# Optimization experiments

Hardware: AMD Instinct MI355X
Metric: run time of the kernel (lower is better)

Reference implementation:

```python
import jax, jax.numpy as jnp
import numpy as np

SIZE = 7  # grid size; H = W = SIZE


def setup_inputs() -> dict:
    key = jax.random.key(0)
    k1, k2, k3, k4 = jax.random.split(key, 4)
    N, C = 256, 2048
    x = jax.random.normal(k1, (N, C, SIZE, SIZE), dtype=jnp.float32)
    mask = jax.random.uniform(k2, (N, SIZE, SIZE), dtype=jnp.float32)
    W = jax.random.normal(k3, (2, 2 * C), dtype=jnp.float32) * 0.02
    b = jax.random.normal(k4, (2,), dtype=jnp.float32) * 0.02
    return {"x": x, "mask": mask, "W": W, "b": b}


def reference(x, mask, W, b):
    N, C, H, Wd = x.shape
    HW = H * Wd
    size = float(H)
    # (N, HW, C) tokens
    reduced_x = jnp.transpose(x.reshape(N, C, HW), (0, 2, 1))
    m = mask.reshape(N, HW)
    thr = jnp.mean(m, axis=1, keepdims=True)  # curr_coef = 1.0
    binary_mask = (m > thr).astype(x.dtype)  # (N, HW)
    # mean over channels of masked tokens, then argmax over positions
    masked_mean = jnp.mean(reduced_x * binary_mask[:, :, None], axis=-1)  # (N, HW)
    max_index = jnp.argmax(masked_mean, axis=-1)  # (N,)
    batch_idx = jnp.arange(N)
    max_features = reduced_x[batch_idx, max_index]  # (N, C)
    # concat(max_feature, token) -> tiny linear 2C -> 2 with ReLU
    disc = jnp.concatenate(
        [jnp.broadcast_to(max_features[:, None, :], (N, HW, C)), reduced_x], axis=-1
    )  # (N, HW, 2C)
    preds_coord = jax.nn.relu(jnp.einsum('npc,oc->npo', disc, W) + b)  # (N, HW, 2)
    # zero out prediction at the anchor position
    preds_coord = preds_coord.at[batch_idx, max_index].set(0.0)
    # polar-coordinate targets relative to anchor
    ii, jj = jnp.meshgrid(jnp.arange(H), jnp.arange(Wd), indexing='ij')
    label = jnp.stack([ii, jj], axis=-1).astype(x.dtype).reshape(HW, 2)  # (HW, 2)
    basic_anchor = label[max_index][:, None, :]  # (N, 1, 2)
    rel = (label[None, :, :] - basic_anchor) / size  # (N, HW, 2)
    relative_dist = jnp.sqrt(jnp.sum(rel ** 2, axis=-1))  # (N, HW)
    relative_angle = jnp.arctan2(rel[:, :, 1], rel[:, :, 0])
    relative_angle = (relative_angle / jnp.float32(np.pi) + 1.0) / 2.0  # (N, HW)
    preds_dist = preds_coord[:, :, 0]
    preds_angle = preds_coord[:, :, 1]
    dist_loss = (preds_dist - relative_dist) ** 2
    gap = preds_angle - relative_angle
    gap = jnp.where(gap < 0, gap + 1.0, gap)
    gap = gap - jnp.mean(gap, axis=-1, keepdims=True)
    angle_loss = gap ** 2
    return (dist_loss + angle_loss).reshape(N, H, Wd)
```

## Files before the change

kernel.cpp:

```cpp
#include <hip/hip_runtime.h>
#include <math.h>

#define N_     256
#define C_     2048
#define HW_    49
#define CHUNKS 4
#define CPB    (C_/CHUNKS)
#define CPW    (CPB/4)
#define NG     5

__global__ __launch_bounds__(256) void k_dot(const float* __restrict__ x,
                                             const float* __restrict__ Wm,
                                             float* __restrict__ part) {
  const int chunk = blockIdx.x;
  const int n     = blockIdx.y;
  const int t     = threadIdx.x;
  const int w     = t >> 6;
  const int l     = t & 63;

  __shared__ float red[4][NG][HW_ + 7];

  const int cbase = chunk*CPB + w*CPW;
  const float* xq   = x + ((size_t)n*C_ + cbase)*HW_ + (l < HW_ ? l : 0);
  const float* w_u0 = Wm + cbase;
  const float* w_u1 = Wm + 2*C_ + cbase;
  const float* w_t0 = Wm + C_ + cbase;
  const float* w_t1 = Wm + 3*C_ + cbase;

  float a0=0.f, a1=0.f, a2=0.f, a3=0.f, a4=0.f;
  #pragma unroll 8
  for (int c = 0; c < CPW; ++c) {
    const float xv = xq[(size_t)c*HW_];
    const float b0 = w_u0[c];
    const float b1 = w_u1[c];
    const float b2 = w_t0[c];
    const float b3 = w_t1[c];
    a0 += xv;
    a1 = fmaf(xv, b0, a1);
    a2 = fmaf(xv, b1, a2);
    a3 = fmaf(xv, b2, a3);
    a4 = fmaf(xv, b3, a4);
  }

  if (l < HW_) {
    red[w][0][l] = a0; red[w][1][l] = a1; red[w][2][l] = a2;
    red[w][3][l] = a3; red[w][4][l] = a4;
  }
  __syncthreads();

  if (t < NG*HW_) {
    const int g = t / HW_, p = t - g*HW_;
    const float s = red[0][g][p] + red[1][g][p] + red[2][g][p] + red[3][g][p];
    part[((size_t)n*CHUNKS + chunk)*(NG*HW_) + t] = s;
  }
}

__global__ __launch_bounds__(256) void k_final(const float* __restrict__ part,
                                               const float* __restrict__ mask,
                                               const float* __restrict__ b,
                                               float* __restrict__ out) {
  const int n = blockIdx.x;
  const int t = threadIdx.x;
  __shared__ float red[NG*HW_];

  if (t < NG*HW_) {
    float a = 0.f;
    #pragma unroll
    for (int ch = 0; ch < CHUNKS; ++ch)
      a += part[((size_t)n*CHUNKS + ch)*(NG*HW_) + t];
    red[t] = a;
  }
  __syncthreads();

  if (t < 64) {
    const int  p   = t;
    const bool act = (p < HW_);

    float m = act ? mask[n*HW_ + p] : 0.f;
    float tot = m;
    #pragma unroll
    for (int off = 32; off; off >>= 1) tot += __shfl_xor(tot, off);
    const float thr = tot / 49.f;

    float s  = act ? red[0*HW_ + p] : 0.f;
    float mm = act ? ((m > thr) ? (s * (1.f/2048.f)) : 0.f) : -INFINITY;
    float best = mm;
    int   bidx = act ? p : 64;
    #pragma unroll
    for (int off = 32; off; off >>= 1) {
      float ov = __shfl_xor(best, off);
      int   oi = __shfl_xor(bidx, off);
      if (ov > best || (ov == best && oi < bidx)) { best = ov; bidx = oi; }
    }
    const int mi = bidx;

    const float u0mi = red[1*HW_ + mi];
    const float u1mi = red[2*HW_ + mi];

    float pred0 = 0.f, pred1 = 0.f;
    if (act) {
      pred0 = fmaxf(u0mi + red[3*HW_ + p] + b[0], 0.f);
      pred1 = fmaxf(u1mi + red[4*HW_ + p] + b[1], 0.f);
      if (p == mi) { pred0 = 0.f; pred1 = 0.f; }
    }

    const int ii = p / 7,  jj = p - ii*7;
    const int ai = mi / 7, aj = mi - ai*7;
    const float ri = (float)(ii - ai) / 7.f;
    const float rj = (float)(jj - aj) / 7.f;
    const float dist = sqrtf(ri*ri + rj*rj);
    const float ang  = (atan2f(rj, ri) / 3.14159274101257324f + 1.f) * 0.5f;

    float gap = pred1 - ang;
    if (gap < 0.f) gap += 1.f;
    float gsum = act ? gap : 0.f;
    #pragma unroll
    for (int off = 32; off; off >>= 1) gsum += __shfl_xor(gsum, off);
    const float gmean = gsum / 49.f;

    if (act) {
      const float dl = pred0 - dist;
      const float ga = gap - gmean;
      out[n*HW_ + p] = dl*dl + ga*ga;
    }
  }
}

extern "C" void kernel_launch(void* const* d_in, const int* in_sizes, int n_in,
                              void* d_out, int out_size, void* d_ws, size_t ws_size,
                              hipStream_t stream) {
  const float* x    = (const float*)d_in[0];
  const float* mask = (const float*)d_in[1];
  const float* Wm   = (const float*)d_in[2];
  const float* b    = (const float*)d_in[3];
  float* out  = (float*)d_out;
  float* part = (float*)d_ws;

  dim3 g1(CHUNKS, N_);
  k_dot<<<g1, 256, 0, stream>>>(x, Wm, part);
  k_final<<<N_, 256, 0, stream>>>(part, mask, b, out);
}
```

Baseline: 167.3 us.

## Fuse dot-product and finalize kernels into one 1024-thread block per sample

Merges the two-kernel pipeline into a single kernel with one 1024-thread block per sample. Sixteen waves split the channels and reduce through shared memory, so the global partial-sum buffer and the second launch go away. The trade-off is fewer blocks (256 instead of 1024), which may lower memory-level parallelism across the GPU for this bandwidth-bound read of x.

```diff
diff --git a/kernel.cpp b/kernel.cpp
--- a/kernel.cpp
+++ b/kernel.cpp
@@ -4,23 +4,25 @@
 #define N_     256
 #define C_     2048
 #define HW_    49
-#define CHUNKS 4
-#define CPB    (C_/CHUNKS)
-#define CPW    (CPB/4)
+#define WAVES  16
+#define CPW    (C_/WAVES)
 #define NG     5
+#define LDW    52
 
-__global__ __launch_bounds__(256) void k_dot(const float* __restrict__ x,
-                                             const float* __restrict__ Wm,
-                                             float* __restrict__ part) {
-  const int chunk = blockIdx.x;
-  const int n     = blockIdx.y;
-  const int t     = threadIdx.x;
-  const int w     = t >> 6;
-  const int l     = t & 63;
+__global__ __launch_bounds__(1024) void k_fused(const float* __restrict__ x,
+                                                const float* __restrict__ mask,
+                                                const float* __restrict__ Wm,
+                                                const float* __restrict__ bias,
+                                                float* __restrict__ out) {
+  const int n = blockIdx.x;
+  const int t = threadIdx.x;
+  const int w = t >> 6;
+  const int l = t & 63;
 
-  __shared__ float red[4][NG][HW_ + 7];
+  __shared__ float red[WAVES][NG][LDW];
+  __shared__ float fin[NG][HW_];
 
-  const int cbase = chunk*CPB + w*CPW;
+  const int cbase = w * CPW;
   const float* xq   = x + ((size_t)n*C_ + cbase)*HW_ + (l < HW_ ? l : 0);
   const float* w_u0 = Wm + cbase;
   const float* w_u1 = Wm + 2*C_ + cbase;
@@ -28,7 +30,7 @@
   const float* w_t1 = Wm + 3*C_ + cbase;
 
   float a0=0.f, a1=0.f, a2=0.f, a3=0.f, a4=0.f;
-  #pragma unroll 8
+  #pragma unroll 16
   for (int c = 0; c < CPW; ++c) {
     const float xv = xq[(size_t)c*HW_];
     const float b0 = w_u0[c];
@@ -50,25 +52,10 @@
 
   if (t < NG*HW_) {
     const int g = t / HW_, p = t - g*HW_;
-    const float s = red[0][g][p] + red[1][g][p] + red[2][g][p] + red[3][g][p];
-    part[((size_t)n*CHUNKS + chunk)*(NG*HW_) + t] = s;
-  }
-}
-
-__global__ __launch_bounds__(256) void k_final(const float* __restrict__ part,
-                                               const float* __restrict__ mask,
-                                               const float* __restrict__ b,
-                                               float* __restrict__ out) {
-  const int n = blockIdx.x;
-  const int t = threadIdx.x;
-  __shared__ float red[NG*HW_];
-
-  if (t < NG*HW_) {
-    float a = 0.f;
+    float s = 0.f;
     #pragma unroll
-    for (int ch = 0; ch < CHUNKS; ++ch)
-      a += part[((size_t)n*CHUNKS + ch)*(NG*HW_) + t];
-    red[t] = a;
+    for (int j = 0; j < WAVES; ++j) s += red[j][g][p];
+    fin[g][p] = s;
   }
   __syncthreads();
 
@@ -82,7 +69,7 @@
     for (int off = 32; off; off >>= 1) tot += __shfl_xor(tot, off);
     const float thr = tot / 49.f;
 
-    float s  = act ? red[0*HW_ + p] : 0.f;
+    float s  = act ? fin[0][p] : 0.f;
     float mm = act ? ((m > thr) ? (s * (1.f/2048.f)) : 0.f) : -INFINITY;
     float best = mm;
     int   bidx = act ? p : 64;
@@ -94,13 +81,13 @@
     }
     const int mi = bidx;
 
-    const float u0mi = red[1*HW_ + mi];
-    const float u1mi = red[2*HW_ + mi];
+    const float u0mi = fin[1][mi];
+    const float u1mi = fin[2][mi];
 
     float pred0 = 0.f, pred1 = 0.f;
     if (act) {
-      pred0 = fmaxf(u0mi + red[3*HW_ + p] + b[0], 0.f);
-      pred1 = fmaxf(u1mi + red[4*HW_ + p] + b[1], 0.f);
+      pred0 = fmaxf(u0mi + fin[3][p] + bias[0], 0.f);
+      pred1 = fmaxf(u1mi + fin[4][p] + bias[1], 0.f);
       if (p == mi) { pred0 = 0.f; pred1 = 0.f; }
     }
 
@@ -133,10 +120,7 @@
   const float* mask = (const float*)d_in[1];
   const float* Wm   = (const float*)d_in[2];
   const float* b    = (const float*)d_in[3];
-  float* out  = (float*)d_out;
-  float* part = (float*)d_ws;
+  float* out = (float*)d_out;
 
-  dim3 g1(CHUNKS, N_);
-  k_dot<<<g1, 256, 0, stream>>>(x, Wm, part);
-  k_final<<<N_, 256, 0, stream>>>(part, mask, b, out);
+  k_fused<<<N_, 1024, 0, stream>>>(x, mask, Wm, b, out);
 }
```

After: 166.6 us. About the same (-0.4%).
